# Kernel tuning notes

Hardware: AMD Instinct MI355X
Metric: run time of the kernel (lower is better)

Reference implementation:

```python
import jax, jax.numpy as jnp
import numpy as np

K = 2  # binary (k-ary) heap-layout tree: children of node j are K*j+1 .. K*j+K

def _levels(N):
    # level of node i in heap layout = floor(log2(i+1)); returns list of index arrays, root level first
    lev = np.floor(np.log2(np.arange(N) + 1)).astype(np.int64)
    depth = int(lev.max()) + 1
    return [np.where(lev == l)[0] for l in range(depth)]

def setup_inputs() -> dict:
    key = jax.random.key(0)
    ks = jax.random.split(key, 9)
    B, N, D = 512, 127, 300
    s = 0.05
    return {
        'x':     jax.random.normal(ks[0], (B, N, D), jnp.float32),
        'Wioux': jax.random.normal(ks[1], (D, 3 * D), jnp.float32) * s,
        'bioux': jax.random.normal(ks[2], (3 * D,), jnp.float32) * s,
        'Wiouh': jax.random.normal(ks[3], (D, 3 * D), jnp.float32) * s,
        'biouh': jax.random.normal(ks[4], (3 * D,), jnp.float32) * s,
        'Wfx':   jax.random.normal(ks[5], (D, D), jnp.float32) * s,
        'bfx':   jax.random.normal(ks[6], (D,), jnp.float32) * s,
        'Wfh':   jax.random.normal(ks[7], (D, D), jnp.float32) * s,
        'bfh':   jax.random.normal(ks[8], (D,), jnp.float32) * s,
    }

def reference(x, Wioux, bioux, Wiouh, biouh, Wfx, bfx, Wfh, bfh):
    # Child-Sum Tree-LSTM, level-synchronous (leaves -> root), batched over B trees.
    B, N, D = x.shape
    levels = _levels(N)
    H = jnp.zeros((B, N, D), x.dtype)
    C = jnp.zeros((B, N, D), x.dtype)
    for idx in reversed(levels):  # process deepest level first
        ch = idx[:, None] * K + 1 + np.arange(K)          # [n, K] child node ids (static)
        valid = jnp.asarray((ch < N), x.dtype)[None, :, :, None]  # [1,n,K,1]
        chc = np.minimum(ch, N - 1)
        ch_h = H[:, chc] * valid                           # [B,n,K,D]; padded children -> 0 (leaf case)
        ch_c = C[:, chc] * valid
        h_sum = ch_h.sum(axis=2)                           # child-sum of hidden states [B,n,D]
        xj = x[:, idx]                                     # [B,n,D]
        iou = xj @ Wioux + bioux + h_sum @ Wiouh + biouh   # [B,n,3D]
        i_g, o_g, u_g = jnp.split(iou, 3, axis=-1)
        i_g = jax.nn.sigmoid(i_g)
        o_g = jax.nn.sigmoid(o_g)
        u_g = jnp.tanh(u_g)
        fx = (xj @ Wfx + bfx)[:, :, None, :]               # broadcast over children
        f = jax.nn.sigmoid(jnp.einsum('bnkd,de->bnke', ch_h, Wfh) + bfh + fx)
        c = i_g * u_g + (f * ch_c).sum(axis=2)             # fc sum; padded ch_c==0
        h = o_g * jnp.tanh(c)
        H = H.at[:, idx].set(h)
        C = C.at[:, idx].set(c)
    return H  # per-node hidden states (contexts); root hidden = H[:, 0]
```

## Files before the change

### kernel.cpp

```cpp
#include <hip/hip_runtime.h>
#include <math.h>

#define DIM 300
#define NN 127
#define KP 320
#define MATSZ (KP*KP)
#define RBSZ 10240
#define SZH 10321920

typedef short bf16x8 __attribute__((ext_vector_type(8)));
typedef float f32x16 __attribute__((ext_vector_type(16)));

__device__ __forceinline__ unsigned short f2bf(float f){
    unsigned u = __float_as_uint(f);
    u += 0x7fffu + ((u >> 16) & 1u);
    return (unsigned short)(u >> 16);
}
__device__ __forceinline__ float sigf(float v){ return 1.0f/(1.0f+__expf(-v)); }
__device__ __forceinline__ float tanh_(float v){
    float t = __expf(-2.0f*fabsf(v));
    float r = (1.0f - t)/(1.0f + t);
    return v < 0.0f ? -r : r;
}

#define MFMA __builtin_amdgcn_mfma_f32_32x32x16_bf16


__global__ void prep_weights(const float* __restrict__ Wioux,
                             const float* __restrict__ Wiouh,
                             const float* __restrict__ Wfx,
                             const float* __restrict__ Wfh,
                             unsigned short* __restrict__ WTF)
{
    int k = threadIdx.x;
    int n = blockIdx.x;
    int m = blockIdx.y;
    float v = 0.f;
    if (k < DIM && n < DIM){
        if (m < 3)       v = Wioux[k*(3*DIM) + m*DIM + n];
        else if (m < 6)  v = Wiouh[k*(3*DIM) + (m-3)*DIM + n];
        else if (m == 6) v = Wfx[k*DIM + n];
        else             v = Wfh[k*DIM + n];
    }
    int dst = m*MATSZ + (n>>5)*RBSZ + (k>>5)*1024 + ((k>>4)&1)*512
            + (((k>>3)&1)*32 + (n&31))*8 + (k&7);
    WTF[dst] = f2bf(v);
}

__global__ void prep_x(const float* __restrict__ x, unsigned short* __restrict__ xF)
{
    int id = blockIdx.x;
    int b = id / NN, j = id - b*NN;
    int lev = 31 - __clz(j + 1);
    int lo = (1 << lev) - 1;
    int r = b*(1 << lev) + (j - lo);
    int rb32 = 16*lo + (r >> 5), ri = r & 31;
    int t = threadIdx.x;
    float v = (t < DIM) ? x[id*DIM + t] : 0.f;
    xF[rb32*RBSZ + (t>>5)*1024 + ((t>>4)&1)*512 + (((t>>3)&1)*32 + ri)*8 + (t&7)] = f2bf(v);
}

__global__ __launch_bounds__(256,2)
void leaf_mfma(const unsigned short* __restrict__ xF,
               const unsigned short* __restrict__ WTF,
               const float* __restrict__ bioux, const float* __restrict__ biouh,
               float* __restrict__ H, float* __restrict__ C,
               unsigned short* __restrict__ hF)
{
    const int t = threadIdx.x, lane = t & 63, wave = t >> 6;
    const int wm = wave >> 1, wn = wave & 1;
    const int grow0 = blockIdx.x*64 + wm*32;
    const int d0 = blockIdx.y*64 + wn*32;

    const unsigned short* ap = xF + (16*63 + (grow0 >> 5))*RBSZ + lane*8;
    const unsigned short* bp = WTF + (d0 >> 5)*RBSZ + lane*8;

    f32x16 aI, aO, aU;
    #pragma unroll
    for (int q = 0; q < 16; q++){ aI[q]=0.f; aO[q]=0.f; aU[q]=0.f; }

    #pragma unroll
    for (int ks = 0; ks < 10; ks++){
        #pragma unroll
        for (int kk = 0; kk < 2; kk++){
            const int off = ks*1024 + kk*512;
            bf16x8 ax = *(const bf16x8*)(ap + off);
            bf16x8 b0 = *(const bf16x8*)(bp + 0*MATSZ + off);
            bf16x8 b1 = *(const bf16x8*)(bp + 1*MATSZ + off);
            bf16x8 b2 = *(const bf16x8*)(bp + 2*MATSZ + off);
            aI = MFMA(ax, b0, aI, 0, 0, 0);
            aO = MFMA(ax, b1, aO, 0, 0, 0);
            aU = MFMA(ax, b2, aU, 0, 0, 0);
        }
    }
    int d = d0 + (lane & 31);
    if (d < DIM){
        float bi  = bioux[d]       + biouh[d];
        float bo_ = bioux[DIM+d]   + biouh[DIM+d];
        float bu  = bioux[2*DIM+d] + biouh[2*DIM+d];
        #pragma unroll
        for (int q = 0; q < 16; q++){
            int grow = grow0 + (q&3) + 8*(q>>2) + 4*(lane>>5);
            int b = grow >> 6, j = 63 + (grow & 63);
            int nb = b*NN + j;
            float iv = sigf (aI[q] + bi);
            float ov = sigf (aO[q] + bo_);
            float uv = tanh_(aU[q] + bu);
            float cv = iv*uv;
            float hv = ov*tanh_(cv);
            C[nb*DIM + d] = cv;
            H[nb*DIM + d] = hv;
            int jp = (j - 1) >> 1, s = 1 - (j & 1);
            int rp = b*32 + (jp - 31);
            int dst = s*SZH + (16*31 + (rp>>5))*RBSZ + (d>>5)*1024 + ((d>>4)&1)*512
                    + (((d>>3)&1)*32 + (rp&31))*8 + (d&7);
            hF[dst] = f2bf(hv);
        }
    }
}

__global__ __launch_bounds__(256,2)
void level_mfma(const unsigned short* __restrict__ xF,
                const unsigned short* __restrict__ hF,
                const unsigned short* __restrict__ WTF,
                const float* __restrict__ bioux, const float* __restrict__ biouh,
                const float* __restrict__ bfx,   const float* __restrict__ bfh,
                float* __restrict__ H, float* __restrict__ C,
                unsigned short* __restrict__ hFw,
                int lshift)
{
    const int t = threadIdx.x, lane = t & 63, wave = t >> 6;
    const int wm = wave >> 1, wn = wave & 1;
    const int grow0 = blockIdx.x*64 + wm*32;
    const int d0 = blockIdx.y*64 + wn*32;
    const int lo = (1 << lshift) - 1;

    const int base32 = 16*lo + (grow0 >> 5);
    const unsigned short* ap  = xF + base32*RBSZ + lane*8;
    const unsigned short* h0p = hF + base32*RBSZ + lane*8;
    const unsigned short* h1p = h0p + SZH;
    const unsigned short* bp  = WTF + (d0 >> 5)*RBSZ + lane*8;

    f32x16 aI, aO, aU, aF0, aF1;
    #pragma unroll
    for (int q = 0; q < 16; q++){
        aI[q]=0.f; aO[q]=0.f; aU[q]=0.f; aF0[q]=0.f; aF1[q]=0.f;
    }

    #pragma unroll
    for (int ks = 0; ks < 10; ks++){
        #pragma unroll
        for (int kk = 0; kk < 2; kk++){
            const int off = ks*1024 + kk*512;
            bf16x8 ax = *(const bf16x8*)(ap  + off);
            bf16x8 a0 = *(const bf16x8*)(h0p + off);
            bf16x8 a1 = *(const bf16x8*)(h1p + off);
            bf16x8 b0 = *(const bf16x8*)(bp + 0*MATSZ + off);
            bf16x8 b1 = *(const bf16x8*)(bp + 1*MATSZ + off);
            bf16x8 b2 = *(const bf16x8*)(bp + 2*MATSZ + off);
            bf16x8 b3 = *(const bf16x8*)(bp + 3*MATSZ + off);
            bf16x8 b4 = *(const bf16x8*)(bp + 4*MATSZ + off);
            bf16x8 b5 = *(const bf16x8*)(bp + 5*MATSZ + off);
            bf16x8 b6 = *(const bf16x8*)(bp + 6*MATSZ + off);
            bf16x8 b7 = *(const bf16x8*)(bp + 7*MATSZ + off);
            aI  = MFMA(ax, b0, aI , 0, 0, 0);
            aI  = MFMA(a0, b3, aI , 0, 0, 0);
            aI  = MFMA(a1, b3, aI , 0, 0, 0);
            aO  = MFMA(ax, b1, aO , 0, 0, 0);
            aO  = MFMA(a0, b4, aO , 0, 0, 0);
            aO  = MFMA(a1, b4, aO , 0, 0, 0);
            aU  = MFMA(ax, b2, aU , 0, 0, 0);
            aU  = MFMA(a0, b5, aU , 0, 0, 0);
            aU  = MFMA(a1, b5, aU , 0, 0, 0);
            aF0 = MFMA(ax, b6, aF0, 0, 0, 0);
            aF0 = MFMA(a0, b7, aF0, 0, 0, 0);
            aF1 = MFMA(ax, b6, aF1, 0, 0, 0);
            aF1 = MFMA(a1, b7, aF1, 0, 0, 0);
        }
    }
    int d = d0 + (lane & 31);
    if (d < DIM){
        float bi  = bioux[d]       + biouh[d];
        float bo_ = bioux[DIM+d]   + biouh[DIM+d];
        float bu  = bioux[2*DIM+d] + biouh[2*DIM+d];
        float bf_ = bfx[d] + bfh[d];
        #pragma unroll
        for (int q = 0; q < 16; q++){
            int grow = grow0 + (q&3) + 8*(q>>2) + 4*(lane>>5);
            int b = grow >> lshift, j = lo + (grow & lo);
            int nb = b*NN + j;
            float c0 = C[(b*NN + 2*j+1)*DIM + d];
            float c1 = C[(b*NN + 2*j+2)*DIM + d];
            float iv = sigf (aI[q] + bi);
            float ov = sigf (aO[q] + bo_);
            float uv = tanh_(aU[q] + bu);
            float f0 = sigf (aF0[q] + bf_);
            float f1 = sigf (aF1[q] + bf_);
            float cv = iv*uv + f0*c0 + f1*c1;
            float hv = ov*tanh_(cv);
            C[nb*DIM + d] = cv;
            H[nb*DIM + d] = hv;
            if (lshift > 0){
                int jp = (j - 1) >> 1, s = 1 - (j & 1);
                int lop = (1 << (lshift-1)) - 1;
                int rp = b*(1 << (lshift-1)) + (jp - lop);
                int dst = s*SZH + (16*lop + (rp>>5))*RBSZ + (d>>5)*1024 + ((d>>4)&1)*512
                        + (((d>>3)&1)*32 + (rp&31))*8 + (d&7);
                hFw[dst] = f2bf(hv);
            }
        }
    }
}

extern "C" void kernel_launch(void* const* d_in, const int* in_sizes, int n_in,
                              void* d_out, int out_size, void* d_ws, size_t ws_size,
                              hipStream_t stream) {
    const float* x     = (const float*)d_in[0];
    const float* Wioux = (const float*)d_in[1];
    const float* bioux = (const float*)d_in[2];
    const float* Wiouh = (const float*)d_in[3];
    const float* biouh = (const float*)d_in[4];
    const float* Wfx   = (const float*)d_in[5];
    const float* bfx   = (const float*)d_in[6];
    const float* Wfh   = (const float*)d_in[7];
    const float* bfh   = (const float*)d_in[8];
    float* H = (float*)d_out;
    float* C = (float*)d_ws;
    unsigned short* WTF = (unsigned short*)((char*)d_ws + 78028800);
    unsigned short* xF  = (unsigned short*)((char*)d_ws + 79667200);
    unsigned short* hF  = (unsigned short*)((char*)d_ws + 121282560);

    hipMemsetAsync(hF, 0, (size_t)SZH*2*2, stream);
    prep_weights<<<dim3(KP, 8), KP, 0, stream>>>(Wioux, Wiouh, Wfx, Wfh, WTF);
    prep_x<<<dim3(512*NN), KP, 0, stream>>>(x, xF);
    leaf_mfma<<<dim3(512, 5), 256, 0, stream>>>(xF, WTF, bioux, biouh, H, C, hF);
    for (int l = 5; l >= 0; l--){
        level_mfma<<<dim3(8 << l, 5), 256, 0, stream>>>(
            xF, hF, WTF, bioux, biouh, bfx, bfh, H, C, hF, l);
    }
}
```

Before: 586.4 us.

## Fuse tail tree levels into one persistent kernel with a grid barrier, prefetch MFMA operands

Levels 3 down to 0 now run in a single 320-block kernel that synchronises between levels through an atomic-counter grid barrier instead of separate launches. The MFMA inner loops in the leaf and level kernels are rewritten with two-stage register double-buffering, so the loads for step s+2 are issued while step s computes. The leaf kernel's launch bound goes from 2 to 3 blocks per CU. The 20 MB memset of the child-hidden buffer is replaced by a 4-byte barrier reset. This relies on every hF slot being written before it is read, and on all 320 blocks being co-resident for the spin barrier to avoid deadlock.

```diff
diff --git a/kernel.cpp b/kernel.cpp
--- a/kernel.cpp
+++ b/kernel.cpp
@@ -32,9 +32,7 @@
                              const float* __restrict__ Wfh,
                              unsigned short* __restrict__ WTF)
 {
-    int k = threadIdx.x;
-    int n = blockIdx.x;
-    int m = blockIdx.y;
+    int k = threadIdx.x, n = blockIdx.x, m = blockIdx.y;
     float v = 0.f;
     if (k < DIM && n < DIM){
         if (m < 3)       v = Wioux[k*(3*DIM) + m*DIM + n];
@@ -60,7 +58,7 @@
     xF[rb32*RBSZ + (t>>5)*1024 + ((t>>4)&1)*512 + (((t>>3)&1)*32 + ri)*8 + (t&7)] = f2bf(v);
 }
 
-__global__ __launch_bounds__(256,2)
+__global__ __launch_bounds__(256,3)
 void leaf_mfma(const unsigned short* __restrict__ xF,
                const unsigned short* __restrict__ WTF,
                const float* __restrict__ bioux, const float* __restrict__ biouh,
@@ -79,19 +77,22 @@
     #pragma unroll
     for (int q = 0; q < 16; q++){ aI[q]=0.f; aO[q]=0.f; aU[q]=0.f; }
 
-    #pragma unroll
-    for (int ks = 0; ks < 10; ks++){
-        #pragma unroll
-        for (int kk = 0; kk < 2; kk++){
-            const int off = ks*1024 + kk*512;
-            bf16x8 ax = *(const bf16x8*)(ap + off);
-            bf16x8 b0 = *(const bf16x8*)(bp + 0*MATSZ + off);
-            bf16x8 b1 = *(const bf16x8*)(bp + 1*MATSZ + off);
-            bf16x8 b2 = *(const bf16x8*)(bp + 2*MATSZ + off);
-            aI = MFMA(ax, b0, aI, 0, 0, 0);
-            aO = MFMA(ax, b1, aO, 0, 0, 0);
-            aU = MFMA(ax, b2, aU, 0, 0, 0);
-        }
+    bf16x8 Af[2]; bf16x8 Bf[2][3];
+    auto loadstep = [&](int buf, int s){
+        const int off = (s>>1)*1024 + (s&1)*512;
+        Af[buf] = *(const bf16x8*)(ap + off);
+        #pragma unroll
+        for (int m = 0; m < 3; m++)
+            Bf[buf][m] = *(const bf16x8*)(bp + m*MATSZ + off);
+    };
+    loadstep(0,0); loadstep(1,1);
+    #pragma unroll
+    for (int s = 0; s < 20; s++){
+        const int cb = s & 1;
+        aI = MFMA(Af[cb], Bf[cb][0], aI, 0, 0, 0);
+        aO = MFMA(Af[cb], Bf[cb][1], aO, 0, 0, 0);
+        aU = MFMA(Af[cb], Bf[cb][2], aU, 0, 0, 0);
+        if (s < 18) loadstep(cb, s+2);
     }
     int d = d0 + (lane & 31);
     if (d < DIM){
@@ -110,29 +111,28 @@
             float hv = ov*tanh_(cv);
             C[nb*DIM + d] = cv;
             H[nb*DIM + d] = hv;
-            int jp = (j - 1) >> 1, s = 1 - (j & 1);
+            int jp = (j - 1) >> 1, s2 = 1 - (j & 1);
             int rp = b*32 + (jp - 31);
-            int dst = s*SZH + (16*31 + (rp>>5))*RBSZ + (d>>5)*1024 + ((d>>4)&1)*512
+            int dst = s2*SZH + (16*31 + (rp>>5))*RBSZ + (d>>5)*1024 + ((d>>4)&1)*512
                     + (((d>>3)&1)*32 + (rp&31))*8 + (d&7);
             hF[dst] = f2bf(hv);
         }
     }
 }
 
-__global__ __launch_bounds__(256,2)
-void level_mfma(const unsigned short* __restrict__ xF,
-                const unsigned short* __restrict__ hF,
-                const unsigned short* __restrict__ WTF,
-                const float* __restrict__ bioux, const float* __restrict__ biouh,
-                const float* __restrict__ bfx,   const float* __restrict__ bfh,
-                float* __restrict__ H, float* __restrict__ C,
-                unsigned short* __restrict__ hFw,
-                int lshift)
-{
-    const int t = threadIdx.x, lane = t & 63, wave = t >> 6;
+__device__ __forceinline__ void level_body(
+    int bx, int by, int lshift,
+    const unsigned short* __restrict__ xF, const unsigned short* __restrict__ hF,
+    const unsigned short* __restrict__ WTF,
+    const float* __restrict__ bioux, const float* __restrict__ biouh,
+    const float* __restrict__ bfx,   const float* __restrict__ bfh,
+    float* __restrict__ H, float* __restrict__ C,
+    unsigned short* __restrict__ hFw,
+    int lane, int wave)
+{
     const int wm = wave >> 1, wn = wave & 1;
-    const int grow0 = blockIdx.x*64 + wm*32;
-    const int d0 = blockIdx.y*64 + wn*32;
+    const int grow0 = bx*64 + wm*32;
+    const int d0 = by*64 + wn*32;
     const int lo = (1 << lshift) - 1;
 
     const int base32 = 16*lo + (grow0 >> 5);
@@ -147,36 +147,34 @@
         aI[q]=0.f; aO[q]=0.f; aU[q]=0.f; aF0[q]=0.f; aF1[q]=0.f;
     }
 
-    #pragma unroll
-    for (int ks = 0; ks < 10; ks++){
-        #pragma unroll
-        for (int kk = 0; kk < 2; kk++){
-            const int off = ks*1024 + kk*512;
-            bf16x8 ax = *(const bf16x8*)(ap  + off);
-            bf16x8 a0 = *(const bf16x8*)(h0p + off);
-            bf16x8 a1 = *(const bf16x8*)(h1p + off);
-            bf16x8 b0 = *(const bf16x8*)(bp + 0*MATSZ + off);
-            bf16x8 b1 = *(const bf16x8*)(bp + 1*MATSZ + off);
-            bf16x8 b2 = *(const bf16x8*)(bp + 2*MATSZ + off);
-            bf16x8 b3 = *(const bf16x8*)(bp + 3*MATSZ + off);
-            bf16x8 b4 = *(const bf16x8*)(bp + 4*MATSZ + off);
-            bf16x8 b5 = *(const bf16x8*)(bp + 5*MATSZ + off);
-            bf16x8 b6 = *(const bf16x8*)(bp + 6*MATSZ + off);
-            bf16x8 b7 = *(const bf16x8*)(bp + 7*MATSZ + off);
-            aI  = MFMA(ax, b0, aI , 0, 0, 0);
-            aI  = MFMA(a0, b3, aI , 0, 0, 0);
-            aI  = MFMA(a1, b3, aI , 0, 0, 0);
-            aO  = MFMA(ax, b1, aO , 0, 0, 0);
-            aO  = MFMA(a0, b4, aO , 0, 0, 0);
-            aO  = MFMA(a1, b4, aO , 0, 0, 0);
-            aU  = MFMA(ax, b2, aU , 0, 0, 0);
-            aU  = MFMA(a0, b5, aU , 0, 0, 0);
-            aU  = MFMA(a1, b5, aU , 0, 0, 0);
-            aF0 = MFMA(ax, b6, aF0, 0, 0, 0);
-            aF0 = MFMA(a0, b7, aF0, 0, 0, 0);
-            aF1 = MFMA(ax, b6, aF1, 0, 0, 0);
-            aF1 = MFMA(a1, b7, aF1, 0, 0, 0);
-        }
+    bf16x8 Af[2][3]; bf16x8 Bf[2][8];
+    auto loadstep = [&](int buf, int s){
+        const int off = (s>>1)*1024 + (s&1)*512;
+        Af[buf][0] = *(const bf16x8*)(ap  + off);
+        Af[buf][1] = *(const bf16x8*)(h0p + off);
+        Af[buf][2] = *(const bf16x8*)(h1p + off);
+        #pragma unroll
+        for (int m = 0; m < 8; m++)
+            Bf[buf][m] = *(const bf16x8*)(bp + m*MATSZ + off);
+    };
+    loadstep(0,0); loadstep(1,1);
+    #pragma unroll
+    for (int s = 0; s < 20; s++){
+        const int cb = s & 1;
+        aI  = MFMA(Af[cb][0], Bf[cb][0], aI , 0, 0, 0);
+        aI  = MFMA(Af[cb][1], Bf[cb][3], aI , 0, 0, 0);
+        aI  = MFMA(Af[cb][2], Bf[cb][3], aI , 0, 0, 0);
+        aO  = MFMA(Af[cb][0], Bf[cb][1], aO , 0, 0, 0);
+        aO  = MFMA(Af[cb][1], Bf[cb][4], aO , 0, 0, 0);
+        aO  = MFMA(Af[cb][2], Bf[cb][4], aO , 0, 0, 0);
+        aU  = MFMA(Af[cb][0], Bf[cb][2], aU , 0, 0, 0);
+        aU  = MFMA(Af[cb][1], Bf[cb][5], aU , 0, 0, 0);
+        aU  = MFMA(Af[cb][2], Bf[cb][5], aU , 0, 0, 0);
+        aF0 = MFMA(Af[cb][0], Bf[cb][6], aF0, 0, 0, 0);
+        aF0 = MFMA(Af[cb][1], Bf[cb][7], aF0, 0, 0, 0);
+        aF1 = MFMA(Af[cb][0], Bf[cb][6], aF1, 0, 0, 0);
+        aF1 = MFMA(Af[cb][2], Bf[cb][7], aF1, 0, 0, 0);
+        if (s < 18) loadstep(cb, s+2);
     }
     int d = d0 + (lane & 31);
     if (d < DIM){
@@ -201,13 +199,65 @@
             C[nb*DIM + d] = cv;
             H[nb*DIM + d] = hv;
             if (lshift > 0){
-                int jp = (j - 1) >> 1, s = 1 - (j & 1);
+                int jp = (j - 1) >> 1, s2 = 1 - (j & 1);
                 int lop = (1 << (lshift-1)) - 1;
                 int rp = b*(1 << (lshift-1)) + (jp - lop);
-                int dst = s*SZH + (16*lop + (rp>>5))*RBSZ + (d>>5)*1024 + ((d>>4)&1)*512
+                int dst = s2*SZH + (16*lop + (rp>>5))*RBSZ + (d>>5)*1024 + ((d>>4)&1)*512
                         + (((d>>3)&1)*32 + (rp&31))*8 + (d&7);
                 hFw[dst] = f2bf(hv);
             }
+        }
+    }
+}
+
+__global__ __launch_bounds__(256,2)
+void level_mfma(const unsigned short* __restrict__ xF,
+                const unsigned short* __restrict__ hF,
+                const unsigned short* __restrict__ WTF,
+                const float* __restrict__ bioux, const float* __restrict__ biouh,
+                const float* __restrict__ bfx,   const float* __restrict__ bfh,
+                float* __restrict__ H, float* __restrict__ C,
+                unsigned short* __restrict__ hFw,
+                int lshift)
+{
+    const int t = threadIdx.x;
+    level_body(blockIdx.x, blockIdx.y, lshift, xF, hF, WTF,
+               bioux, biouh, bfx, bfh, H, C, hFw, t & 63, t >> 6);
+}
+
+__global__ __launch_bounds__(256,2)
+void tail_mfma(const unsigned short* __restrict__ xF,
+               const unsigned short* __restrict__ hF,
+               const unsigned short* __restrict__ WTF,
+               const float* __restrict__ bioux, const float* __restrict__ biouh,
+               const float* __restrict__ bfx,   const float* __restrict__ bfh,
+               float* __restrict__ H, float* __restrict__ C,
+               unsigned short* __restrict__ hFw,
+               unsigned int* bar)
+{
+    const int t = threadIdx.x;
+    const int lane = t & 63, wave = t >> 6;
+    int phase = 0;
+    for (int l = 3; l >= 0; l--){
+        const int nx = 8 << l;
+        if ((int)blockIdx.x < nx*5){
+            int bx = blockIdx.x % nx, by = blockIdx.x / nx;
+            level_body(bx, by, l, xF, hF, WTF, bioux, biouh, bfx, bfh,
+                       H, C, hFw, lane, wave);
+        }
+        if (l > 0){
+            __threadfence();
+            __syncthreads();
+            if (t == 0){
+                atomicAdd(bar, 1u);
+                unsigned target = 320u * (unsigned)(phase + 1);
+                while (atomicAdd(bar, 0u) < target){
+                    __builtin_amdgcn_s_sleep(8);
+                }
+            }
+            __syncthreads();
+            __threadfence();
+            phase++;
         }
     }
 }
@@ -229,13 +279,16 @@
     unsigned short* WTF = (unsigned short*)((char*)d_ws + 78028800);
     unsigned short* xF  = (unsigned short*)((char*)d_ws + 79667200);
     unsigned short* hF  = (unsigned short*)((char*)d_ws + 121282560);
-
-    hipMemsetAsync(hF, 0, (size_t)SZH*2*2, stream);
+    unsigned int*   bar = (unsigned int*)((char*)d_ws + 162570240);
+
+    hipMemsetAsync(bar, 0, 4, stream);
     prep_weights<<<dim3(KP, 8), KP, 0, stream>>>(Wioux, Wiouh, Wfx, Wfh, WTF);
     prep_x<<<dim3(512*NN), KP, 0, stream>>>(x, xF);
     leaf_mfma<<<dim3(512, 5), 256, 0, stream>>>(xF, WTF, bioux, biouh, H, C, hF);
-    for (int l = 5; l >= 0; l--){
+    for (int l = 5; l >= 4; l--){
         level_mfma<<<dim3(8 << l, 5), 256, 0, stream>>>(
             xF, hF, WTF, bioux, biouh, bfx, bfh, H, C, hF, l);
     }
-}
+    tail_mfma<<<dim3(320), 256, 0, stream>>>(
+        xF, hF, WTF, bioux, biouh, bfx, bfh, H, C, hF, bar);
+}
```

Result: slower. 764.7 us (+30.4%).
